# Kernel tuning notes

Hardware: AMD Instinct MI355X
Metric: run time of the kernel (lower is better)

The kernel has to match this reference:

```python
import jax, jax.numpy as jnp
import numpy as np

TEMPERATURE = 298.0
SG_HASH = 16  # hashings.atom_hash['CYS']['SG']
COL_BATCH, COL_CHAIN, COL_RESNUM, COL_ATNAME = 0, 1, 2, 3
N_BATCH, N_CHAIN, N_RES = 2, 4, 50000  # static (= runtime max+1 in the torch code)


def setup_inputs() -> dict:
    N, P, A, APR = 500_000, 8_000_000, 4, 10  # atoms, pairs, alternatives, atoms-per-residue
    key = jax.random.key(0)
    ks = jax.random.split(key, 8)
    coords = jax.random.normal(ks[0], (N, 3), dtype=jnp.float32) * 10.0
    at_name = jax.random.randint(ks[1], (N,), 0, 32)
    resnum = jnp.arange(N) // APR  # N_RES = N // APR residues
    batch = jax.random.randint(ks[2], (N,), 0, N_BATCH)
    chain = jax.random.randint(ks[3], (N,), 0, N_CHAIN)
    atom_description = jnp.stack([batch, chain, resnum, at_name], axis=1)
    p0 = jax.random.randint(ks[4], (P,), 0, N)
    off = jax.random.randint(ks[5], (P,), APR, N - APR)  # ensures resnum[p0] != resnum[p1]
    atomPairs = jnp.stack([p0, (p0 + off) % N], axis=1)
    alternativeMask = jax.random.randint(ks[6], (N, A), 0, 2).astype(bool)
    atom_number = jnp.arange(N)
    partners = jnp.zeros((N,), dtype=jnp.int32)
    facc = jax.random.uniform(ks[7], (N,), dtype=jnp.float32)
    return dict(coords=coords, atom_description=atom_description, atom_number=atom_number,
                atomPairs=atomPairs, alternativeMask=alternativeMask, partners=partners, facc=facc)


def reference(coords, atom_description, atom_number, atomPairs, alternativeMask, partners, facc):
    p0, p1 = atomPairs[:, 0], atomPairs[:, 1]
    at_name = atom_description[:, COL_ATNAME]
    sulfur = (at_name[p0] == SG_HASH) & (at_name[p1] == SG_HASH)  # [P] bool; disulfNetwork mask
    # torch.pairwise_distance adds eps=1e-6 to the difference before the norm
    diff = coords[p0] - coords[p1] + 1e-6
    dist = jnp.sqrt(jnp.sum(diff * diff, axis=-1))  # [P]
    resnum = atom_description[:, COL_RESNUM]
    rd = jnp.abs(resnum[p0] - resnum[p1]).astype(jnp.float32)
    safe_rd = jnp.where(sulfur, rd, 1.0)  # keep log finite off the sulfur mask
    energy = -0.001 * TEMPERATURE * (2.1 + 2.9823825 * jnp.log(safe_rd)) + 5.0 * jnp.abs(dist - 2.04)
    netE = jnp.where(sulfur, 0.5 * energy, 0.0)  # masked, halved pair energy [P]
    # bindToAtoms: per-alternative masked scatter-add to both endpoints (vectorized over alts)
    pair_alt = alternativeMask[p0] & alternativeMask[p1]  # [P, A]
    contrib = jnp.where(pair_alt, netE[:, None], 0.0)  # [P, A]
    N, A = alternativeMask.shape
    atomEnergy = jnp.zeros((N, A), jnp.float32).at[p0].add(contrib).at[p1].add(contrib)
    # bindToResi: scatter-add atom energies to (batch, chain, resnum) bins
    flat = (atom_description[:, COL_BATCH] * N_CHAIN + atom_description[:, COL_CHAIN]) * N_RES + resnum
    residueEnergy = jax.ops.segment_sum(atomEnergy, flat, num_segments=N_BATCH * N_CHAIN * N_RES)
    residueEnergy = residueEnergy.reshape(N_BATCH, N_CHAIN, N_RES, A)
    return residueEnergy, atomEnergy, sulfur
```

## Files before the change

### kernel.cpp

```cpp
#include <hip/hip_runtime.h>

#define N_ATOMS   500000
#define N_ALT     4
#define NB        2
#define NC        4
#define NR        50000
#define SG_HASH   16
#define TEMP      298.0f

#define RESE_SIZE  (NB * NC * NR * N_ALT)
#define ATOME_SIZE (N_ATOMS * N_ALT)
#define ZERO_F4    ((RESE_SIZE + ATOME_SIZE) / 4)

#define MASK_W64   ((N_ATOMS + 63) / 64)
#define MASK_W32   (MASK_W64 * 2)

__global__ __launch_bounds__(1024) void prep_kernel(
    const int* __restrict__ adesc,
    float* __restrict__ zero_base,
    unsigned long long* __restrict__ mask)
{
    int i = blockIdx.x * 1024 + threadIdx.x;

    if (i < ZERO_F4)
        reinterpret_cast<float4*>(zero_base)[i] = make_float4(0.f, 0.f, 0.f, 0.f);

    bool s = false;
    if (i < N_ATOMS) s = (adesc[(size_t)i * 4 + 3] == SG_HASH);
    unsigned long long b = __ballot(s);
    if (i < N_ATOMS && (threadIdx.x & 63) == 0) mask[i >> 6] = b;
}

__device__ __forceinline__ void heavy_pair(
    int p0, int p1,
    const float* __restrict__ coords,
    const int*   __restrict__ adesc,
    const int*   __restrict__ altmask,
    float* __restrict__ resE,
    float* __restrict__ atomE)
{
    int4 d0 = *reinterpret_cast<const int4*>(adesc + (size_t)p0 * 4);
    int4 d1 = *reinterpret_cast<const int4*>(adesc + (size_t)p1 * 4);

    float dx = coords[(size_t)p0 * 3 + 0] - coords[(size_t)p1 * 3 + 0] + 1e-6f;
    float dy = coords[(size_t)p0 * 3 + 1] - coords[(size_t)p1 * 3 + 1] + 1e-6f;
    float dz = coords[(size_t)p0 * 3 + 2] - coords[(size_t)p1 * 3 + 2] + 1e-6f;
    float dist = sqrtf(dx * dx + dy * dy + dz * dz);

    float rd = fabsf((float)(d0.z - d1.z));
    float energy = -0.001f * TEMP * (2.1f + 2.9823825f * logf(rd))
                 + 5.0f * fabsf(dist - 2.04f);
    float netE = 0.5f * energy;

    int4 m0 = *reinterpret_cast<const int4*>(altmask + (size_t)p0 * 4);
    int4 m1 = *reinterpret_cast<const int4*>(altmask + (size_t)p1 * 4);

    int f0 = ((d0.x * NC + d0.y) * NR + d0.z) * N_ALT;
    int f1 = ((d1.x * NC + d1.y) * NR + d1.z) * N_ALT;

    const int* m0p = &m0.x;
    const int* m1p = &m1.x;
#pragma unroll
    for (int a = 0; a < N_ALT; ++a) {
        if (m0p[a] & m1p[a]) {
            atomicAdd(atomE + (size_t)p0 * N_ALT + a, netE);
            atomicAdd(atomE + (size_t)p1 * N_ALT + a, netE);
            atomicAdd(resE + f0 + a, netE);
            atomicAdd(resE + f1 + a, netE);
        }
    }
}

__device__ __forceinline__ bool probe2(const unsigned int* __restrict__ lm,
                                       int a, int b) {
    unsigned m = (lm[a >> 5] >> (a & 31)) & (lm[b >> 5] >> (b & 31));
    return m & 1u;
}

__global__ __launch_bounds__(1024) void disulfide_pair_kernel(
    const float* __restrict__ coords,
    const int*   __restrict__ adesc,
    const int*   __restrict__ pairs,
    const int*   __restrict__ altmask,
    const unsigned int* __restrict__ sgmask32,
    float* __restrict__ resE,
    float* __restrict__ atomE,
    float* __restrict__ sulfur,
    int P)
{
    __shared__ unsigned int lmask[MASK_W32];

    for (int w = threadIdx.x; w < MASK_W32; w += 1024)
        lmask[w] = sgmask32[w];
    __syncthreads();

    const int tid    = blockIdx.x * 1024 + threadIdx.x;
    const int stride = gridDim.x * 1024 * 8;

    for (int i0 = tid * 8; i0 < P; i0 += stride) {
        const int4* pp = reinterpret_cast<const int4*>(pairs + (size_t)i0 * 2);
        int4 pa = pp[0];
        int4 pb = pp[1];
        int4 pc = pp[2];
        int4 pd = pp[3];

        bool s0 = probe2(lmask, pa.x, pa.y);
        bool s1 = probe2(lmask, pa.z, pa.w);
        bool s2 = probe2(lmask, pb.x, pb.y);
        bool s3 = probe2(lmask, pb.z, pb.w);
        bool s4 = probe2(lmask, pc.x, pc.y);
        bool s5 = probe2(lmask, pc.z, pc.w);
        bool s6 = probe2(lmask, pd.x, pd.y);
        bool s7 = probe2(lmask, pd.z, pd.w);

        float4 sv0 = make_float4(s0 ? 1.0f : 0.0f, s1 ? 1.0f : 0.0f,
                                 s2 ? 1.0f : 0.0f, s3 ? 1.0f : 0.0f);
        float4 sv1 = make_float4(s4 ? 1.0f : 0.0f, s5 ? 1.0f : 0.0f,
                                 s6 ? 1.0f : 0.0f, s7 ? 1.0f : 0.0f);
        float4* sp = reinterpret_cast<float4*>(sulfur + i0);
        sp[0] = sv0;
        sp[1] = sv1;

        if (s0) heavy_pair(pa.x, pa.y, coords, adesc, altmask, resE, atomE);
        if (s1) heavy_pair(pa.z, pa.w, coords, adesc, altmask, resE, atomE);
        if (s2) heavy_pair(pb.x, pb.y, coords, adesc, altmask, resE, atomE);
        if (s3) heavy_pair(pb.z, pb.w, coords, adesc, altmask, resE, atomE);
        if (s4) heavy_pair(pc.x, pc.y, coords, adesc, altmask, resE, atomE);
        if (s5) heavy_pair(pc.z, pc.w, coords, adesc, altmask, resE, atomE);
        if (s6) heavy_pair(pd.x, pd.y, coords, adesc, altmask, resE, atomE);
        if (s7) heavy_pair(pd.z, pd.w, coords, adesc, altmask, resE, atomE);
    }
}

extern "C" void kernel_launch(void* const* d_in, const int* in_sizes, int n_in,
                              void* d_out, int out_size, void* d_ws, size_t ws_size,
                              hipStream_t stream) {
    const float* coords  = (const float*)d_in[0];
    const int*   adesc   = (const int*)d_in[1];
    const int*   pairs   = (const int*)d_in[3];
    const int*   altmask = (const int*)d_in[4];

    const int P = in_sizes[3] / 2;

    float* out    = (float*)d_out;
    float* resE   = out;
    float* atomE  = out + RESE_SIZE;
    float* sulfur = out + RESE_SIZE + ATOME_SIZE;

    unsigned long long* sgmask = (unsigned long long*)d_ws;

    {
        const int threads = 1024;
        const int blocks  = (ZERO_F4 + threads - 1) / threads;
        prep_kernel<<<blocks, threads, 0, stream>>>(adesc, resE, sgmask);
    }

    {
        const int threads = 1024;
        const int blocks  = 512;
        disulfide_pair_kernel<<<blocks, threads, 0, stream>>>(
            coords, adesc, pairs, altmask, (const unsigned int*)sgmask,
            resE, atomE, sulfur, P);
    }
}
```

Measured before the change: 29.39 us.

## Fuse prep and pair kernels into one cooperative kernel with grid sync

Merges the output-zeroing and sulfur-mask-building prep kernel into the pair kernel, using a cooperative launch and a grid-wide barrier between the phases. This removes one kernel launch and its launch gap. In exchange it adds a grid sync plus an occupancy query on the host every call. The grid size is capped by occupancy, so zeroing is done with a grid-stride loop.

```diff
diff --git a/kernel.cpp b/kernel.cpp
--- a/kernel.cpp
+++ b/kernel.cpp
@@ -1,4 +1,7 @@
 #include <hip/hip_runtime.h>
+#include <hip/hip_cooperative_groups.h>
+
+namespace cg = cooperative_groups;
 
 #define N_ATOMS   500000
 #define N_ALT     4
@@ -14,22 +17,7 @@
 
 #define MASK_W64   ((N_ATOMS + 63) / 64)
 #define MASK_W32   (MASK_W64 * 2)
-
-__global__ __launch_bounds__(1024) void prep_kernel(
-    const int* __restrict__ adesc,
-    float* __restrict__ zero_base,
-    unsigned long long* __restrict__ mask)
-{
-    int i = blockIdx.x * 1024 + threadIdx.x;
-
-    if (i < ZERO_F4)
-        reinterpret_cast<float4*>(zero_base)[i] = make_float4(0.f, 0.f, 0.f, 0.f);
-
-    bool s = false;
-    if (i < N_ATOMS) s = (adesc[(size_t)i * 4 + 3] == SG_HASH);
-    unsigned long long b = __ballot(s);
-    if (i < N_ATOMS && (threadIdx.x & 63) == 0) mask[i >> 6] = b;
-}
+#define MASK_V4    ((MASK_W32 + 3) / 4)
 
 __device__ __forceinline__ void heavy_pair(
     int p0, int p1,
@@ -77,26 +65,43 @@
     return m & 1u;
 }
 
-__global__ __launch_bounds__(1024) void disulfide_pair_kernel(
+__global__ __launch_bounds__(1024) void disulfide_fused_kernel(
     const float* __restrict__ coords,
     const int*   __restrict__ adesc,
     const int*   __restrict__ pairs,
     const int*   __restrict__ altmask,
-    const unsigned int* __restrict__ sgmask32,
+    unsigned long long* __restrict__ gmask,
     float* __restrict__ resE,
     float* __restrict__ atomE,
     float* __restrict__ sulfur,
     int P)
 {
-    __shared__ unsigned int lmask[MASK_W32];
+    __shared__ unsigned int lmask[MASK_V4 * 4];
 
-    for (int w = threadIdx.x; w < MASK_W32; w += 1024)
-        lmask[w] = sgmask32[w];
+    const int nthreads = gridDim.x * 1024;
+    const int tid      = blockIdx.x * 1024 + threadIdx.x;
+    const int lane     = threadIdx.x & 63;
+
+    for (int i = tid; i < ZERO_F4; i += nthreads)
+        reinterpret_cast<float4*>(resE)[i] = make_float4(0.f, 0.f, 0.f, 0.f);
+
+    for (int i = tid; (i - lane) < N_ATOMS; i += nthreads) {
+        bool s = (i < N_ATOMS) && (adesc[(size_t)i * 4 + 3] == SG_HASH);
+        unsigned long long b = __ballot(s);
+        if (lane == 0 && i < N_ATOMS) gmask[i >> 6] = b;
+    }
+
+    cg::this_grid().sync();
+
+    {
+        const uint4* g4 = reinterpret_cast<const uint4*>(gmask);
+        uint4* l4 = reinterpret_cast<uint4*>(lmask);
+        for (int w = threadIdx.x; w < MASK_V4; w += 1024)
+            l4[w] = g4[w];
+    }
     __syncthreads();
 
-    const int tid    = blockIdx.x * 1024 + threadIdx.x;
-    const int stride = gridDim.x * 1024 * 8;
-
+    const int stride = nthreads * 8;
     for (int i0 = tid * 8; i0 < P; i0 += stride) {
         const int4* pp = reinterpret_cast<const int4*>(pairs + (size_t)i0 * 2);
         int4 pa = pp[0];
@@ -140,26 +145,26 @@
     const int*   pairs   = (const int*)d_in[3];
     const int*   altmask = (const int*)d_in[4];
 
-    const int P = in_sizes[3] / 2;
+    int P = in_sizes[3] / 2;
 
     float* out    = (float*)d_out;
     float* resE   = out;
     float* atomE  = out + RESE_SIZE;
     float* sulfur = out + RESE_SIZE + ATOME_SIZE;
 
-    unsigned long long* sgmask = (unsigned long long*)d_ws;
+    unsigned long long* gmask = (unsigned long long*)d_ws;
 
-    {
-        const int threads = 1024;
-        const int blocks  = (ZERO_F4 + threads - 1) / threads;
-        prep_kernel<<<blocks, threads, 0, stream>>>(adesc, resE, sgmask);
-    }
+    int maxBlocksPerCU = 0;
+    hipError_t e = hipOccupancyMaxActiveBlocksPerMultiprocessor(
+        &maxBlocksPerCU, disulfide_fused_kernel, 1024, 0);
+    if (e != hipSuccess || maxBlocksPerCU < 1) maxBlocksPerCU = 1;
+    int blocks = maxBlocksPerCU * 256;
+    if (blocks > 512) blocks = 512;
 
-    {
-        const int threads = 1024;
-        const int blocks  = 512;
-        disulfide_pair_kernel<<<blocks, threads, 0, stream>>>(
-            coords, adesc, pairs, altmask, (const unsigned int*)sgmask,
-            resE, atomE, sulfur, P);
-    }
+    void* args[] = {
+        (void*)&coords, (void*)&adesc, (void*)&pairs, (void*)&altmask,
+        (void*)&gmask, (void*)&resE, (void*)&atomE, (void*)&sulfur, (void*)&P
+    };
+    hipLaunchCooperativeKernel(disulfide_fused_kernel,
+                               dim3(blocks), dim3(1024), args, 0, stream);
 }
```

Measured after the change: 66.00 us. +124.5%, slower.
